# Performance work log

Measured on AMD Instinct MI355X. Metric: run time of the kernel, lower is better.

The kernel has to match this reference:

```python
import jax, jax.numpy as jnp
import numpy as np

EMBED_DIM = 1024
NUM_HEADS = 16
HEAD_DIM = EMBED_DIM // NUM_HEADS
SCALE = 1.0 / float(np.sqrt(HEAD_DIM))


def setup_inputs() -> dict:
    key = jax.random.key(0)
    ks = jax.random.split(key, 5)
    B, S, E = 2, 2048, EMBED_DIM
    x = jax.random.normal(ks[0], (B, S, E), dtype=jnp.float32)
    # nn.Linear-style params (weights stored [out, in] in torch; we keep [in, out] for x @ W)
    w_qkv = jax.random.normal(ks[1], (E, 3 * E), dtype=jnp.float32) / np.sqrt(E)
    b_qkv = jax.random.normal(ks[2], (3 * E,), dtype=jnp.float32) * 0.02
    w_out = jax.random.normal(ks[3], (E, E), dtype=jnp.float32) / np.sqrt(E)
    b_out = jax.random.normal(ks[4], (E,), dtype=jnp.float32) * 0.02
    return {"x": x, "w_qkv": w_qkv, "b_qkv": b_qkv, "w_out": w_out, "b_out": b_out}


def reference(x, w_qkv, b_qkv, w_out, b_out) -> jnp.ndarray:
    B, S, E = x.shape
    H, Dh = NUM_HEADS, HEAD_DIM
    # fused QKV projection
    qkv = x @ w_qkv + b_qkv                                  # [B, S, 3E]
    qkv = qkv.reshape(B, S, 3, H, Dh)
    qkv = jnp.transpose(qkv, (2, 0, 3, 1, 4))                # [3, B, H, S, Dh]
    q, k, v = qkv[0], qkv[1], qkv[2]
    # naive attention (matches _local_attention), is_causal=True
    scores = jnp.einsum('bhqd,bhkd->bhqk', q, k) * SCALE      # [B, H, S, S]
    causal = jnp.triu(jnp.full((S, S), -jnp.inf, dtype=scores.dtype), k=1)
    scores = scores + causal
    attn = jax.nn.softmax(scores, axis=-1)
    out = jnp.einsum('bhqk,bhkd->bhqd', attn, v)              # [B, H, S, Dh]
    out = jnp.transpose(out, (0, 2, 1, 3)).reshape(B, S, E)
    return out @ w_out + b_out
```

## Files before the change

kernel.cpp:

```cpp
#include <hip/hip_runtime.h>
#include <math.h>

static constexpr int Ee  = 1024;
static constexpr int Ss  = 2048;
static constexpr int Bb  = 2;
static constexpr int Hh  = 16;
static constexpr int DHd = 64;
static constexpr int Mm  = Bb * Ss;
static constexpr int Kk  = 1024;

typedef __attribute__((ext_vector_type(8))) short short8;
typedef __attribute__((ext_vector_type(4))) float f32x4;


__device__ __forceinline__ unsigned short f2bf(float f) {
    unsigned u = __float_as_uint(f);
    u += 0x7fffu + ((u >> 16) & 1u);
    return (unsigned short)(u >> 16);
}
__device__ __forceinline__ float bf2f(unsigned short h) {
    return __uint_as_float(((unsigned)h) << 16);
}
__device__ __forceinline__ void hilo(float f, unsigned short& h, unsigned short& l) {
    h = f2bf(f);
    l = f2bf(f - bf2f(h));
}

__global__ __launch_bounds__(256) void cvt_x_packed(
    const float* __restrict__ in, unsigned short* __restrict__ outp)
{
    const int i   = blockIdx.x * 256 + threadIdx.x;
    const int row = i >> 7;
    const int ki  = i & 127;
    const int kb  = ki >> 2;
    const int gl  = ki & 3;
    const float4 v0 = *(const float4*)&in[(size_t)row * 1024 + ki * 8];
    const float4 v1 = *(const float4*)&in[(size_t)row * 1024 + ki * 8 + 4];
    const float f[8] = {v0.x, v0.y, v0.z, v0.w, v1.x, v1.y, v1.z, v1.w};
    short8 hv, lv;
    #pragma unroll
    for (int j = 0; j < 8; ++j) {
        unsigned short h, l;
        hilo(f[j], h, l);
        hv[j] = (short)h;
        lv[j] = (short)l;
    }
    unsigned short* base = outp + (size_t)row * 2048 + kb * 64;
    const int sw = row & 7;
    *(short8*)(base + ((gl ^ sw) << 3))       = hv;
    *(short8*)(base + (((gl | 4) ^ sw) << 3)) = lv;
}

__global__ __launch_bounds__(256) void cvt_w_packed(
    const float* __restrict__ W, unsigned short* __restrict__ Wp, int N)
{
    __shared__ float tile[32][65];
    const int kb = blockIdx.x;
    const int n0 = blockIdx.y * 64;
    const int k0 = kb * 32;
    const int t  = threadIdx.x;
    {
        const int kr = t >> 4, nc = t & 15;
        #pragma unroll
        for (int i = 0; i < 2; ++i) {
            const int k = kr + i * 16;
            float4 v = *(const float4*)&W[(size_t)(k0 + k) * N + n0 + nc * 4];
            tile[k][nc * 4 + 0] = v.x;
            tile[k][nc * 4 + 1] = v.y;
            tile[k][nc * 4 + 2] = v.z;
            tile[k][nc * 4 + 3] = v.w;
        }
    }
    __syncthreads();
    const int n  = t >> 2;
    const int gl = t & 3;
    const int ng = n0 + n;
    short8 hv, lv;
    #pragma unroll
    for (int j = 0; j < 8; ++j) {
        unsigned short h, l;
        hilo(tile[gl * 8 + j][n], h, l);
        hv[j] = (short)h;
        lv[j] = (short)l;
    }
    unsigned short* base = Wp + (size_t)ng * 2048 + kb * 64;
    const int sw = ng & 7;
    *(short8*)(base + ((gl ^ sw) << 3))       = hv;
    *(short8*)(base + (((gl | 4) ^ sw) << 3)) = lv;
}

template <int N, bool QKV>
__global__ __launch_bounds__(256) void gemm_bf16x3(
    const unsigned short* __restrict__ Ap, const unsigned short* __restrict__ Bp,
    const float* __restrict__ bias, float* __restrict__ O0,
    unsigned short* __restrict__ Qh, unsigned short* __restrict__ Ql,
    unsigned short* __restrict__ Kh, unsigned short* __restrict__ Kl,
    unsigned short* __restrict__ Vh, unsigned short* __restrict__ Vl)
{
    __shared__ __align__(16) unsigned short As[128 * 64];
    __shared__ __align__(16) unsigned short Bs[128 * 64];

    const int t  = threadIdx.x;
    const int m0 = blockIdx.y * 128, n0 = blockIdx.x * 128;
    const int w  = t >> 6, lane = t & 63;
    const int wr = w >> 1, wc = w & 1;
    const int lr = lane & 15, lk = lane >> 4;
    const int sw = lr & 7;

    f32x4 acc[4][4] = {};

    #pragma unroll 1
    for (int kb = 0; kb < 32; ++kb) {
        #pragma unroll
        for (int i = 0; i < 4; ++i) {
            const int seg = t + i * 256;
            const int row = seg >> 3, gp = seg & 7;
            const size_t goA = (size_t)(m0 + row) * 2048 + kb * 64 + gp * 8;
            const size_t goB = (size_t)(n0 + row) * 2048 + kb * 64 + gp * 8;
            const int lo = (i * 256 + (t & ~63)) * 8;
            __builtin_amdgcn_global_load_lds(
                (const __attribute__((address_space(1))) void*)(Ap + goA),
                (__attribute__((address_space(3))) void*)(As + lo), 16, 0, 0);
            __builtin_amdgcn_global_load_lds(
                (const __attribute__((address_space(1))) void*)(Bp + goB),
                (__attribute__((address_space(3))) void*)(Bs + lo), 16, 0, 0);
        }
        __syncthreads();

        short8 avh[4], avl[4], bvh[4], bvl[4];
        #pragma unroll
        for (int m = 0; m < 4; ++m) {
            const int rb = (wr * 64 + m * 16 + lr) * 64;
            avh[m] = *(const short8*)&As[rb + ((lk ^ sw) << 3)];
            avl[m] = *(const short8*)&As[rb + (((lk | 4) ^ sw) << 3)];
        }
        #pragma unroll
        for (int n = 0; n < 4; ++n) {
            const int rb = (wc * 64 + n * 16 + lr) * 64;
            bvh[n] = *(const short8*)&Bs[rb + ((lk ^ sw) << 3)];
            bvl[n] = *(const short8*)&Bs[rb + (((lk | 4) ^ sw) << 3)];
        }
        #pragma unroll
        for (int m = 0; m < 4; ++m)
            #pragma unroll
            for (int n = 0; n < 4; ++n) {
                acc[m][n] = __builtin_amdgcn_mfma_f32_16x16x32_bf16(
                    avh[m], bvh[n], acc[m][n], 0, 0, 0);
                acc[m][n] = __builtin_amdgcn_mfma_f32_16x16x32_bf16(
                    avh[m], bvl[n], acc[m][n], 0, 0, 0);
                acc[m][n] = __builtin_amdgcn_mfma_f32_16x16x32_bf16(
                    avl[m], bvh[n], acc[m][n], 0, 0, 0);
            }
        __syncthreads();
    }

    #pragma unroll
    for (int n = 0; n < 4; ++n) {
        const int gcol = n0 + wc * 64 + n * 16 + lr;
        const float bb = bias[gcol];
        if (QKV) {
            const int c  = gcol >> 10;
            const int hd = (gcol >> 6) & 15;
            const int d  = gcol & 63;
            #pragma unroll
            for (int m = 0; m < 4; ++m) {
                #pragma unroll
                for (int r = 0; r < 4; ++r) {
                    const int grow = m0 + wr * 64 + m * 16 + lk * 4 + r;
                    const int b = grow >> 11, s = grow & (Ss - 1);
                    const int bh = b * Hh + hd;
                    const int kv = s & 63;
                    float v = acc[m][n][r] + bb;
                    if (c == 0) v *= 0.125f;
                    unsigned short vh_, vl_;
                    hilo(v, vh_, vl_);
                    size_t off;
                    unsigned short *ph, *pl;
                    if (c == 0) {
                        off = ((size_t)bh * Ss + s) * 64 + d;
                        ph = Qh; pl = Ql;
                    } else if (c == 1) {
                        off = (size_t)bh * 131072 + (size_t)(s >> 6) * 4096 +
                              kv * 64 + (d ^ ((kv & 7) << 3));
                        ph = Kh; pl = Kl;
                    } else {
                        off = (size_t)bh * 131072 + (size_t)(s >> 6) * 4096 +
                              d * 64 + (kv ^ ((d & 7) << 3));
                        ph = Vh; pl = Vl;
                    }
                    ph[off] = vh_;
                    pl[off] = vl_;
                }
            }
        } else {
            #pragma unroll
            for (int m = 0; m < 4; ++m) {
                #pragma unroll
                for (int r = 0; r < 4; ++r) {
                    const int grow = m0 + wr * 64 + m * 16 + lk * 4 + r;
                    O0[(size_t)grow * N + gcol] = acc[m][n][r] + bb;
                }
            }
        }
    }
}

__global__ __launch_bounds__(256, 4) void flash_mfma(
    const unsigned short* __restrict__ Qgh, const unsigned short* __restrict__ Qgl,
    const unsigned short* __restrict__ Kgh, const unsigned short* __restrict__ Kgl,
    const unsigned short* __restrict__ Vgh, const unsigned short* __restrict__ Vgl,
    unsigned short* __restrict__ AOp)
{
    __shared__ __align__(16) unsigned short Ksh[4096], Ksl[4096];
    __shared__ __align__(16) unsigned short Vsh[4096], Vsl[4096];
    __shared__ __align__(16) unsigned short Ph[4096], Pl[4096];

    const int t    = threadIdx.x;
    const int w    = t >> 6, lane = t & 63;
    const int lr   = lane & 15, g = lane >> 4;
    const int bid  = blockIdx.x;
    const int qt   = 31 - (bid >> 5);
    const int bh   = bid & 31;
    const int b    = bh >> 4, h = bh & 15;
    const int q0   = qt * 64;
    const int wq0  = w * 16;
    const int qloc = wq0 + lr;
    const int qg   = q0 + qloc;

    short8 qbh[2], qbl[2];
    #pragma unroll
    for (int ks = 0; ks < 2; ++ks) {
        const size_t off = ((size_t)bh * Ss + qg) * 64 + ks * 32 + g * 8;
        qbh[ks] = *(const short8*)&Qgh[off];
        qbl[ks] = *(const short8*)&Qgl[off];
    }

    f32x4 o[4] = {};
    float lp = 0.f;
    const int swq = (lr & 7) << 3;

    const int nkt = qt + 1;
    #pragma unroll 1
    for (int kt = 0; kt < nkt; ++kt) {
        const size_t gb = ((size_t)bh * 32 + kt) * 4096;
        #pragma unroll
        for (int i = 0; i < 2; ++i) {
            const int seg = i * 256 + t;
            const int lo = (i * 256 + (t & ~63)) * 8;
            __builtin_amdgcn_global_load_lds(
                (const __attribute__((address_space(1))) void*)(Kgh + gb + seg * 8),
                (__attribute__((address_space(3))) void*)(Ksh + lo), 16, 0, 0);
            __builtin_amdgcn_global_load_lds(
                (const __attribute__((address_space(1))) void*)(Kgl + gb + seg * 8),
                (__attribute__((address_space(3))) void*)(Ksl + lo), 16, 0, 0);
            __builtin_amdgcn_global_load_lds(
                (const __attribute__((address_space(1))) void*)(Vgh + gb + seg * 8),
                (__attribute__((address_space(3))) void*)(Vsh + lo), 16, 0, 0);
            __builtin_amdgcn_global_load_lds(
                (const __attribute__((address_space(1))) void*)(Vgl + gb + seg * 8),
                (__attribute__((address_space(3))) void*)(Vsl + lo), 16, 0, 0);
        }
        __syncthreads();

        f32x4 s[4] = {};
        #pragma unroll
        for (int ks = 0; ks < 2; ++ks) {
            const int d0 = ks * 32 + g * 8;
            #pragma unroll
            for (int n = 0; n < 4; ++n) {
                const int kv = n * 16 + lr;
                const int idx = kv * 64 + (d0 ^ ((kv & 7) << 3));
                const short8 kh = *(const short8*)&Ksh[idx];
                const short8 kl = *(const short8*)&Ksl[idx];
                s[n] = __builtin_amdgcn_mfma_f32_16x16x32_bf16(kh, qbh[ks], s[n], 0, 0, 0);
                s[n] = __builtin_amdgcn_mfma_f32_16x16x32_bf16(kh, qbl[ks], s[n], 0, 0, 0);
                s[n] = __builtin_amdgcn_mfma_f32_16x16x32_bf16(kl, qbh[ks], s[n], 0, 0, 0);
            }
        }

        if (kt == qt) {
            #pragma unroll
            for (int n = 0; n < 4; ++n)
                #pragma unroll
                for (int r = 0; r < 4; ++r) {
                    const int kv = kt * 64 + n * 16 + g * 4 + r;
                    if (kv > qg) s[n][r] = -INFINITY;
                }
        }

        #pragma unroll
        for (int n = 0; n < 4; ++n) {
            const float p0 = exp2f(fmaf(s[n][0], 1.44269504f, -23.0831184f));
            const float p1 = exp2f(fmaf(s[n][1], 1.44269504f, -23.0831184f));
            const float p2 = exp2f(fmaf(s[n][2], 1.44269504f, -23.0831184f));
            const float p3 = exp2f(fmaf(s[n][3], 1.44269504f, -23.0831184f));
            lp += (p0 + p1) + (p2 + p3);
            const unsigned a0 = __float_as_uint(p0), a1 = __float_as_uint(p1);
            const unsigned a2 = __float_as_uint(p2), a3 = __float_as_uint(p3);
            uint2 uh, ul;
            uh.x = (a0 >> 16) | (a1 & 0xffff0000u);
            uh.y = (a2 >> 16) | (a3 & 0xffff0000u);
            const float r0 = p0 - __uint_as_float(a0 & 0xffff0000u);
            const float r1 = p1 - __uint_as_float(a1 & 0xffff0000u);
            const float r2 = p2 - __uint_as_float(a2 & 0xffff0000u);
            const float r3 = p3 - __uint_as_float(a3 & 0xffff0000u);
            ul.x = (__float_as_uint(r0) >> 16) | (__float_as_uint(r1) & 0xffff0000u);
            ul.y = (__float_as_uint(r2) >> 16) | (__float_as_uint(r3) & 0xffff0000u);
            const int kv0 = n * 16 + g * 4;
            const int idx = qloc * 64 + (kv0 ^ swq);
            *(uint2*)&Ph[idx] = uh;
            *(uint2*)&Pl[idx] = ul;
        }

        #pragma unroll
        for (int ks = 0; ks < 2; ++ks) {
            const int kv0 = ks * 32 + g * 8;
            const int pidx = qloc * 64 + (kv0 ^ swq);
            const short8 pah = *(const short8*)&Ph[pidx];
            const short8 pal = *(const short8*)&Pl[pidx];
            #pragma unroll
            for (int df = 0; df < 4; ++df) {
                const int d = df * 16 + lr;
                const int vidx = d * 64 + (kv0 ^ ((d & 7) << 3));
                const short8 vh_ = *(const short8*)&Vsh[vidx];
                const short8 vl_ = *(const short8*)&Vsl[vidx];
                o[df] = __builtin_amdgcn_mfma_f32_16x16x32_bf16(pah, vh_, o[df], 0, 0, 0);
                o[df] = __builtin_amdgcn_mfma_f32_16x16x32_bf16(pah, vl_, o[df], 0, 0, 0);
                o[df] = __builtin_amdgcn_mfma_f32_16x16x32_bf16(pal, vh_, o[df], 0, 0, 0);
            }
        }
        __syncthreads();
    }

    lp += __shfl_xor(lp, 16);
    lp += __shfl_xor(lp, 32);
    float linv[4];
    #pragma unroll
    for (int r = 0; r < 4; ++r)
        linv[r] = 1.f / __shfl(lp, g * 4 + r);

    #pragma unroll
    for (int df = 0; df < 4; ++df) {
        const int k = h * 64 + df * 16 + lr;
        const int kb2 = k >> 5, gl = (k >> 3) & 3, el = k & 7;
        #pragma unroll
        for (int r = 0; r < 4; ++r) {
            const int q = q0 + wq0 + g * 4 + r;
            const int m = b * Ss + q;
            const float v = o[df][r] * linv[r];
            const unsigned a = __float_as_uint(v);
            const unsigned short hh = (unsigned short)(a >> 16);
            const float rr = v - __uint_as_float(a & 0xffff0000u);
            const unsigned short ll = (unsigned short)(__float_as_uint(rr) >> 16);
            unsigned short* bse = AOp + (size_t)m * 2048 + kb2 * 64;
            const int sw = m & 7;
            bse[((gl ^ sw) << 3) + el]       = hh;
            bse[(((gl | 4) ^ sw) << 3) + el] = ll;
        }
    }
}

extern "C" void kernel_launch(void* const* d_in, const int* in_sizes, int n_in,
                              void* d_out, int out_size, void* d_ws, size_t ws_size,
                              hipStream_t stream)
{
    const float* x     = (const float*)d_in[0];
    const float* w_qkv = (const float*)d_in[1];
    const float* b_qkv = (const float*)d_in[2];
    const float* w_out = (const float*)d_in[3];
    const float* b_out = (const float*)d_in[4];
    float* out = (float*)d_out;

    char* wsb = (char*)d_ws;
    const size_t MB = 1024ull * 1024ull;
    unsigned short* Qh  = (unsigned short*)(wsb + 0 * MB);
    unsigned short* Ql  = (unsigned short*)(wsb + 8 * MB);
    unsigned short* Kh  = (unsigned short*)(wsb + 16 * MB);
    unsigned short* Kl  = (unsigned short*)(wsb + 24 * MB);
    unsigned short* Vh  = (unsigned short*)(wsb + 32 * MB);
    unsigned short* Vl  = (unsigned short*)(wsb + 40 * MB);
    unsigned short* Xp  = (unsigned short*)(wsb + 48 * MB);
    unsigned short* AOp = (unsigned short*)(wsb + 48 * MB);
    unsigned short* Wqkvp = (unsigned short*)(wsb + 64 * MB);
    unsigned short* Woutp = (unsigned short*)(wsb + 76 * MB);

    cvt_x_packed<<<2048, 256, 0, stream>>>(x, Xp);
    cvt_w_packed<<<dim3(32, 3072 / 64), 256, 0, stream>>>(w_qkv, Wqkvp, 3072);
    cvt_w_packed<<<dim3(32, 1024 / 64), 256, 0, stream>>>(w_out, Woutp, 1024);

    gemm_bf16x3<3072, true><<<dim3(3072 / 128, Mm / 128), 256, 0, stream>>>(
        Xp, Wqkvp, b_qkv, nullptr, Qh, Ql, Kh, Kl, Vh, Vl);

    flash_mfma<<<dim3(1024), 256, 0, stream>>>(
        Qh, Ql, Kh, Kl, Vh, Vl, AOp);

    gemm_bf16x3<1024, false><<<dim3(1024 / 128, Mm / 128), 256, 0, stream>>>(
        AOp, Woutp, b_out, out,
        nullptr, nullptr, nullptr, nullptr, nullptr, nullptr);
}
```

Before: 300.2 us.

## Use 256x256 double-buffered 8-wave QKV GEMM with direct global-to-LDS loads

```diff
diff --git a/kernel.cpp b/kernel.cpp
--- a/kernel.cpp
+++ b/kernel.cpp
@@ -89,14 +89,134 @@
     *(short8*)(base + (((gl | 4) ^ sw) << 3)) = lv;
 }
 
-template <int N, bool QKV>
-__global__ __launch_bounds__(256) void gemm_bf16x3(
+__global__ __launch_bounds__(512, 2) void gemm_qkv_8w(
     const unsigned short* __restrict__ Ap, const unsigned short* __restrict__ Bp,
-    const float* __restrict__ bias, float* __restrict__ O0,
+    const float* __restrict__ bias,
     unsigned short* __restrict__ Qh, unsigned short* __restrict__ Ql,
     unsigned short* __restrict__ Kh, unsigned short* __restrict__ Kl,
     unsigned short* __restrict__ Vh, unsigned short* __restrict__ Vl)
 {
+    __shared__ __align__(16) unsigned short As[2][256 * 64];
+    __shared__ __align__(16) unsigned short Bs[2][256 * 64];
+
+    const int t    = threadIdx.x;
+    const int m0   = blockIdx.y * 256, n0 = blockIdx.x * 256;
+    const int w    = t >> 6, lane = t & 63;
+    const int wr   = w >> 2, wc = w & 3;
+    const int lr   = lane & 15, lk = lane >> 4;
+    const int sw   = lr & 7;
+    const int wb16 = (t & ~63) * 8;
+
+    f32x4 acc[8][4] = {};
+
+#define STAGE(KB, BUF)                                                         \
+    {                                                                          \
+        const int kb_ = (KB);                                                  \
+        _Pragma("unroll")                                                      \
+        for (int i = 0; i < 4; ++i) {                                          \
+            const int seg = i * 512 + t;                                       \
+            const int row = seg >> 3, gp = seg & 7;                            \
+            const int lo = i * 512 * 8 + wb16;                                 \
+            __builtin_amdgcn_global_load_lds(                                  \
+                (const __attribute__((address_space(1))) void*)                \
+                    (Ap + (size_t)(m0 + row) * 2048 + kb_ * 64 + gp * 8),      \
+                (__attribute__((address_space(3))) void*)(&As[BUF][lo]),       \
+                16, 0, 0);                                                     \
+            __builtin_amdgcn_global_load_lds(                                  \
+                (const __attribute__((address_space(1))) void*)                \
+                    (Bp + (size_t)(n0 + row) * 2048 + kb_ * 64 + gp * 8),      \
+                (__attribute__((address_space(3))) void*)(&Bs[BUF][lo]),       \
+                16, 0, 0);                                                     \
+        }                                                                      \
+    }
+
+    STAGE(0, 0);
+    __syncthreads();
+
+    #pragma unroll 1
+    for (int kb = 0; kb < 32; ++kb) {
+        const int cur = kb & 1;
+        if (kb < 31) STAGE(kb + 1, cur ^ 1);
+        __builtin_amdgcn_sched_barrier(0);
+
+        short8 bvh[4], bvl[4];
+        #pragma unroll
+        for (int n = 0; n < 4; ++n) {
+            const int rb = (wc * 64 + n * 16 + lr) * 64;
+            bvh[n] = *(const short8*)&Bs[cur][rb + ((lk ^ sw) << 3)];
+            bvl[n] = *(const short8*)&Bs[cur][rb + (((lk | 4) ^ sw) << 3)];
+        }
+        #pragma unroll
+        for (int half = 0; half < 2; ++half) {
+            short8 avh[4], avl[4];
+            #pragma unroll
+            for (int m = 0; m < 4; ++m) {
+                const int rb = (wr * 128 + (half * 4 + m) * 16 + lr) * 64;
+                avh[m] = *(const short8*)&As[cur][rb + ((lk ^ sw) << 3)];
+                avl[m] = *(const short8*)&As[cur][rb + (((lk | 4) ^ sw) << 3)];
+            }
+            __builtin_amdgcn_s_setprio(1);
+            #pragma unroll
+            for (int m = 0; m < 4; ++m)
+                #pragma unroll
+                for (int n = 0; n < 4; ++n) {
+                    f32x4 a = acc[half * 4 + m][n];
+                    a = __builtin_amdgcn_mfma_f32_16x16x32_bf16(avh[m], bvh[n], a, 0, 0, 0);
+                    a = __builtin_amdgcn_mfma_f32_16x16x32_bf16(avh[m], bvl[n], a, 0, 0, 0);
+                    a = __builtin_amdgcn_mfma_f32_16x16x32_bf16(avl[m], bvh[n], a, 0, 0, 0);
+                    acc[half * 4 + m][n] = a;
+                }
+            __builtin_amdgcn_s_setprio(0);
+        }
+        __syncthreads();
+    }
+#undef STAGE
+
+    #pragma unroll
+    for (int n = 0; n < 4; ++n) {
+        const int gcol = n0 + wc * 64 + n * 16 + lr;
+        const float bb = bias[gcol];
+        const int c  = gcol >> 10;
+        const int hd = (gcol >> 6) & 15;
+        const int d  = gcol & 63;
+        #pragma unroll
+        for (int m = 0; m < 8; ++m) {
+            #pragma unroll
+            for (int r = 0; r < 4; ++r) {
+                const int grow = m0 + wr * 128 + m * 16 + lk * 4 + r;
+                const int b = grow >> 11, s = grow & (Ss - 1);
+                const int bh = b * Hh + hd;
+                const int kv = s & 63;
+                float v = acc[m][n][r] + bb;
+                if (c == 0) v *= 0.125f;
+                unsigned short vh_, vl_;
+                hilo(v, vh_, vl_);
+                size_t off;
+                unsigned short *ph, *pl;
+                if (c == 0) {
+                    off = ((size_t)bh * Ss + s) * 64 + d;
+                    ph = Qh; pl = Ql;
+                } else if (c == 1) {
+                    off = (size_t)bh * 131072 + (size_t)(s >> 6) * 4096 +
+                          kv * 64 + (d ^ ((kv & 7) << 3));
+                    ph = Kh; pl = Kl;
+                } else {
+                    off = (size_t)bh * 131072 + (size_t)(s >> 6) * 4096 +
+                          d * 64 + (kv ^ ((d & 7) << 3));
+                    ph = Vh; pl = Vl;
+                }
+                ph[off] = vh_;
+                pl[off] = vl_;
+            }
+        }
+    }
+}
+
+__global__ __launch_bounds__(256) void gemm_out(
+    const unsigned short* __restrict__ Ap, const unsigned short* __restrict__ Bp,
+    const float* __restrict__ bias, float* __restrict__ O0)
+{
+    constexpr int N = 1024;
     __shared__ __align__(16) unsigned short As[128 * 64];
     __shared__ __align__(16) unsigned short Bs[128 * 64];
 
@@ -158,48 +278,12 @@
     for (int n = 0; n < 4; ++n) {
         const int gcol = n0 + wc * 64 + n * 16 + lr;
         const float bb = bias[gcol];
-        if (QKV) {
-            const int c  = gcol >> 10;
-            const int hd = (gcol >> 6) & 15;
-            const int d  = gcol & 63;
-            #pragma unroll
-            for (int m = 0; m < 4; ++m) {
-                #pragma unroll
-                for (int r = 0; r < 4; ++r) {
-                    const int grow = m0 + wr * 64 + m * 16 + lk * 4 + r;
-                    const int b = grow >> 11, s = grow & (Ss - 1);
-                    const int bh = b * Hh + hd;
-                    const int kv = s & 63;
-                    float v = acc[m][n][r] + bb;
-                    if (c == 0) v *= 0.125f;
-                    unsigned short vh_, vl_;
-                    hilo(v, vh_, vl_);
-                    size_t off;
-                    unsigned short *ph, *pl;
-                    if (c == 0) {
-                        off = ((size_t)bh * Ss + s) * 64 + d;
-                        ph = Qh; pl = Ql;
-                    } else if (c == 1) {
-                        off = (size_t)bh * 131072 + (size_t)(s >> 6) * 4096 +
-                              kv * 64 + (d ^ ((kv & 7) << 3));
-                        ph = Kh; pl = Kl;
-                    } else {
-                        off = (size_t)bh * 131072 + (size_t)(s >> 6) * 4096 +
-                              d * 64 + (kv ^ ((d & 7) << 3));
-                        ph = Vh; pl = Vl;
-                    }
-                    ph[off] = vh_;
-                    pl[off] = vl_;
-                }
-            }
-        } else {
-            #pragma unroll
-            for (int m = 0; m < 4; ++m) {
-                #pragma unroll
-                for (int r = 0; r < 4; ++r) {
-                    const int grow = m0 + wr * 64 + m * 16 + lk * 4 + r;
-                    O0[(size_t)grow * N + gcol] = acc[m][n][r] + bb;
-                }
+        #pragma unroll
+        for (int m = 0; m < 4; ++m) {
+            #pragma unroll
+            for (int r = 0; r < 4; ++r) {
+                const int grow = m0 + wr * 64 + m * 16 + lk * 4 + r;
+                O0[(size_t)grow * N + gcol] = acc[m][n][r] + bb;
             }
         }
     }
@@ -388,13 +472,12 @@
     cvt_w_packed<<<dim3(32, 3072 / 64), 256, 0, stream>>>(w_qkv, Wqkvp, 3072);
     cvt_w_packed<<<dim3(32, 1024 / 64), 256, 0, stream>>>(w_out, Woutp, 1024);
 
-    gemm_bf16x3<3072, true><<<dim3(3072 / 128, Mm / 128), 256, 0, stream>>>(
-        Xp, Wqkvp, b_qkv, nullptr, Qh, Ql, Kh, Kl, Vh, Vl);
+    gemm_qkv_8w<<<dim3(3072 / 256, Mm / 256), 512, 0, stream>>>(
+        Xp, Wqkvp, b_qkv, Qh, Ql, Kh, Kl, Vh, Vl);
 
     flash_mfma<<<dim3(1024), 256, 0, stream>>>(
         Qh, Ql, Kh, Kl, Vh, Vl, AOp);
 
-    gemm_bf16x3<1024, false><<<dim3(1024 / 128, Mm / 128), 256, 0, stream>>>(
-        AOp, Woutp, b_out, out,
-        nullptr, nullptr, nullptr, nullptr, nullptr, nullptr);
-}
+    gemm_out<<<dim3(1024 / 128, Mm / 128), 256, 0, stream>>>(
+        AOp, Woutp, b_out, out);
+}
```

After: 305.7 us. Within noise of the previous version (+1.8%).

## Pipeline GEMM with triple-buffered LDS ring and 512-thread blocks

Applied to the files above, without the earlier changes.

```diff
diff --git a/kernel.cpp b/kernel.cpp
--- a/kernel.cpp
+++ b/kernel.cpp
@@ -1,5 +1,6 @@
 #include <hip/hip_runtime.h>
 #include <math.h>
+#include <stdint.h>
 
 static constexpr int Ee  = 1024;
 static constexpr int Ss  = 2048;
@@ -90,73 +91,108 @@
 }
 
 template <int N, bool QKV>
-__global__ __launch_bounds__(256) void gemm_bf16x3(
+__global__ __launch_bounds__(512, 2) void gemm_ring(
     const unsigned short* __restrict__ Ap, const unsigned short* __restrict__ Bp,
     const float* __restrict__ bias, float* __restrict__ O0,
     unsigned short* __restrict__ Qh, unsigned short* __restrict__ Ql,
     unsigned short* __restrict__ Kh, unsigned short* __restrict__ Kl,
     unsigned short* __restrict__ Vh, unsigned short* __restrict__ Vl)
 {
-    __shared__ __align__(16) unsigned short As[128 * 64];
-    __shared__ __align__(16) unsigned short Bs[128 * 64];
+    __shared__ __align__(16) unsigned short As[3][128 * 64];
+    __shared__ __align__(16) unsigned short Bs[3][128 * 64];
 
     const int t  = threadIdx.x;
     const int m0 = blockIdx.y * 128, n0 = blockIdx.x * 128;
     const int w  = t >> 6, lane = t & 63;
-    const int wr = w >> 1, wc = w & 1;
+    const int wr = w >> 2, wc = w & 3;
     const int lr = lane & 15, lk = lane >> 4;
     const int sw = lr & 7;
 
-    f32x4 acc[4][4] = {};
-
+    const unsigned aLds = (unsigned)(uintptr_t)
+        (__attribute__((address_space(3))) unsigned short*)&As[0][0];
+    const unsigned bLds = (unsigned)(uintptr_t)
+        (__attribute__((address_space(3))) unsigned short*)&Bs[0][0];
+
+    f32x4 acc[4][2] = {};
+
+#define STAGE(KB, BUF)                                                        \
+    {                                                                         \
+        const int kb_ = (KB), buf_ = (BUF);                                   \
+        _Pragma("unroll")                                                     \
+        for (int i = 0; i < 2; ++i) {                                         \
+            const int seg = i * 512 + t;                                      \
+            const int row = seg >> 3, gp = seg & 7;                           \
+            const int lo = buf_ * 8192 + (i * 512 + (t & ~63)) * 8;           \
+            __builtin_amdgcn_global_load_lds(                                 \
+                (const __attribute__((address_space(1))) void*)               \
+                    (Ap + (size_t)(m0 + row) * 2048 + kb_ * 64 + gp * 8),     \
+                (__attribute__((address_space(3))) void*)(&As[0][0] + lo),    \
+                16, 0, 0);                                                    \
+            __builtin_amdgcn_global_load_lds(                                 \
+                (const __attribute__((address_space(1))) void*)               \
+                    (Bp + (size_t)(n0 + row) * 2048 + kb_ * 64 + gp * 8),     \
+                (__attribute__((address_space(3))) void*)(&Bs[0][0] + lo),    \
+                16, 0, 0);                                                    \
+        }                                                                     \
+    }
+
+    auto step = [&](int cur) {
+        const unsigned abase = aLds + cur * 16384u;
+        const unsigned bbase = bLds + cur * 16384u;
+        short8 avh[4], avl[4], bvh[2], bvl[2];
+        #pragma unroll
+        for (int m = 0; m < 4; ++m) {
+            const unsigned rb = abase + (unsigned)((wr * 64 + m * 16 + lr) * 64) * 2u;
+            const unsigned ah = rb + (unsigned)(((lk ^ sw) << 3) * 2);
+            const unsigned al = rb + (unsigned)((((lk | 4) ^ sw) << 3) * 2);
+            asm volatile("ds_read_b128 %0, %1" : "=&v"(avh[m]) : "v"(ah));
+            asm volatile("ds_read_b128 %0, %1" : "=&v"(avl[m]) : "v"(al));
+        }
+        #pragma unroll
+        for (int n = 0; n < 2; ++n) {
+            const unsigned rb = bbase + (unsigned)((wc * 32 + n * 16 + lr) * 64) * 2u;
+            const unsigned bh = rb + (unsigned)(((lk ^ sw) << 3) * 2);
+            const unsigned bl = rb + (unsigned)((((lk | 4) ^ sw) << 3) * 2);
+            asm volatile("ds_read_b128 %0, %1" : "=&v"(bvh[n]) : "v"(bh));
+            asm volatile("ds_read_b128 %0, %1" : "=&v"(bvl[n]) : "v"(bl));
+        }
+        asm volatile("s_waitcnt lgkmcnt(0)" ::: "memory");
+        __builtin_amdgcn_sched_barrier(0);
+        __builtin_amdgcn_s_setprio(1);
+        #pragma unroll
+        for (int m = 0; m < 4; ++m)
+            #pragma unroll
+            for (int n = 0; n < 2; ++n) {
+                f32x4 a = acc[m][n];
+                a = __builtin_amdgcn_mfma_f32_16x16x32_bf16(avh[m], bvh[n], a, 0, 0, 0);
+                a = __builtin_amdgcn_mfma_f32_16x16x32_bf16(avh[m], bvl[n], a, 0, 0, 0);
+                a = __builtin_amdgcn_mfma_f32_16x16x32_bf16(avl[m], bvh[n], a, 0, 0, 0);
+                acc[m][n] = a;
+            }
+        __builtin_amdgcn_s_setprio(0);
+    };
+
+    STAGE(0, 0);
+    STAGE(1, 1);
+
+    int cur = 0, nxt = 2;
     #pragma unroll 1
-    for (int kb = 0; kb < 32; ++kb) {
-        #pragma unroll
-        for (int i = 0; i < 4; ++i) {
-            const int seg = t + i * 256;
-            const int row = seg >> 3, gp = seg & 7;
-            const size_t goA = (size_t)(m0 + row) * 2048 + kb * 64 + gp * 8;
-            const size_t goB = (size_t)(n0 + row) * 2048 + kb * 64 + gp * 8;
-            const int lo = (i * 256 + (t & ~63)) * 8;
-            __builtin_amdgcn_global_load_lds(
-                (const __attribute__((address_space(1))) void*)(Ap + goA),
-                (__attribute__((address_space(3))) void*)(As + lo), 16, 0, 0);
-            __builtin_amdgcn_global_load_lds(
-                (const __attribute__((address_space(1))) void*)(Bp + goB),
-                (__attribute__((address_space(3))) void*)(Bs + lo), 16, 0, 0);
-        }
-        __syncthreads();
-
-        short8 avh[4], avl[4], bvh[4], bvl[4];
-        #pragma unroll
-        for (int m = 0; m < 4; ++m) {
-            const int rb = (wr * 64 + m * 16 + lr) * 64;
-            avh[m] = *(const short8*)&As[rb + ((lk ^ sw) << 3)];
-            avl[m] = *(const short8*)&As[rb + (((lk | 4) ^ sw) << 3)];
-        }
-        #pragma unroll
-        for (int n = 0; n < 4; ++n) {
-            const int rb = (wc * 64 + n * 16 + lr) * 64;
-            bvh[n] = *(const short8*)&Bs[rb + ((lk ^ sw) << 3)];
-            bvl[n] = *(const short8*)&Bs[rb + (((lk | 4) ^ sw) << 3)];
-        }
-        #pragma unroll
-        for (int m = 0; m < 4; ++m)
-            #pragma unroll
-            for (int n = 0; n < 4; ++n) {
-                acc[m][n] = __builtin_amdgcn_mfma_f32_16x16x32_bf16(
-                    avh[m], bvh[n], acc[m][n], 0, 0, 0);
-                acc[m][n] = __builtin_amdgcn_mfma_f32_16x16x32_bf16(
-                    avh[m], bvl[n], acc[m][n], 0, 0, 0);
-                acc[m][n] = __builtin_amdgcn_mfma_f32_16x16x32_bf16(
-                    avl[m], bvh[n], acc[m][n], 0, 0, 0);
-            }
-        __syncthreads();
-    }
-
-    #pragma unroll
-    for (int n = 0; n < 4; ++n) {
-        const int gcol = n0 + wc * 64 + n * 16 + lr;
+    for (int kb = 0; kb < 31; ++kb) {
+        asm volatile("s_waitcnt vmcnt(4)" ::: "memory");
+        __builtin_amdgcn_s_barrier();
+        if (kb <= 29) STAGE(kb + 2, nxt);
+        step(cur);
+        cur = (cur == 2) ? 0 : cur + 1;
+        nxt = (nxt == 2) ? 0 : nxt + 1;
+    }
+    asm volatile("s_waitcnt vmcnt(0)" ::: "memory");
+    __builtin_amdgcn_s_barrier();
+    step(cur);
+#undef STAGE
+
+    #pragma unroll
+    for (int n = 0; n < 2; ++n) {
+        const int gcol = n0 + wc * 32 + n * 16 + lr;
         const float bb = bias[gcol];
         if (QKV) {
             const int c  = gcol >> 10;
@@ -388,13 +424,13 @@
     cvt_w_packed<<<dim3(32, 3072 / 64), 256, 0, stream>>>(w_qkv, Wqkvp, 3072);
     cvt_w_packed<<<dim3(32, 1024 / 64), 256, 0, stream>>>(w_out, Woutp, 1024);
 
-    gemm_bf16x3<3072, true><<<dim3(3072 / 128, Mm / 128), 256, 0, stream>>>(
+    gemm_ring<3072, true><<<dim3(3072 / 128, Mm / 128), 512, 0, stream>>>(
         Xp, Wqkvp, b_qkv, nullptr, Qh, Ql, Kh, Kl, Vh, Vl);
 
     flash_mfma<<<dim3(1024), 256, 0, stream>>>(
         Qh, Ql, Kh, Kl, Vh, Vl, AOp);
 
-    gemm_bf16x3<1024, false><<<dim3(1024 / 128, Mm / 128), 256, 0, stream>>>(
+    gemm_ring<1024, false><<<dim3(1024 / 128, Mm / 128), 512, 0, stream>>>(
         AOp, Woutp, b_out, out,
         nullptr, nullptr, nullptr, nullptr, nullptr, nullptr);
 }
```

New measurement: 274.9 us. 1.09x faster.
